# Performance work log

Measured on AMD Instinct MI355X. Metric: run time of the kernel, lower is better.

The kernel has to match this reference:

```python
import jax, jax.numpy as jnp
import numpy as np
from jax import lax

# dims
B = 1024          # batch
C_IN = 8          # board feature planes
HW = 8            # board side
FN = 16           # filter_num
SEN, INT, OUT = 1024, 2048, 1024
TOT = SEN + INT + OUT            # 4096
CNN_OUT = sum((HW - k + 1) ** 2 for k in range(1, 9)) * FN  # 204*FN = 3264
NUM_OUT = 1968
LORA_R = 64
LORA_SCALE = 128.0 / LORA_R      # alpha / rank = 2.0
TIMESTEPS = 5
DENSITY = 0.3


def setup_inputs() -> dict:
    key = jax.random.key(0)
    ks = jax.random.split(key, 20)
    inp = {"x": jax.random.normal(ks[0], (B, HW, HW, C_IN), dtype=jnp.float32)}
    # conv bank: kernels 1..8, OIHW layout
    for i, k in enumerate(range(1, 9)):
        inp[f"conv_w{k}"] = jax.random.normal(ks[1 + i], (FN, C_IN, k, k), dtype=jnp.float32) * (1.0 / np.sqrt(C_IN * k * k))
    inp["conv_b"] = jnp.zeros((8, FN), dtype=jnp.float32)
    # recurrent weight with sparsity pattern (mask = W != 0, as in register_buffer('sparsity_mask', W_init != 0))
    Wd = jax.random.normal(ks[9], (TOT, TOT), dtype=jnp.float32) * 0.02
    mask = (jax.random.uniform(ks[10], (TOT, TOT)) < DENSITY).astype(jnp.float32)
    inp["W"] = Wd * mask
    inp["lora_A"] = jax.random.normal(ks[11], (TOT, LORA_R), dtype=jnp.float32) * 0.02
    inp["lora_B"] = jax.random.normal(ks[12], (LORA_R, TOT), dtype=jnp.float32) * 0.02
    inp["ip_w"] = jax.random.normal(ks[13], (CNN_OUT, SEN), dtype=jnp.float32) * (1.0 / np.sqrt(CNN_OUT))
    inp["ip_b"] = jnp.zeros((SEN,), dtype=jnp.float32)
    inp["out_w"] = jax.random.normal(ks[14], (OUT, NUM_OUT), dtype=jnp.float32) * (1.0 / np.sqrt(OUT))
    inp["out_b"] = jnp.zeros((NUM_OUT,), dtype=jnp.float32)
    return inp


def _forward(x, conv_w1, conv_w2, conv_w3, conv_w4, conv_w5, conv_w6, conv_w7, conv_w8,
             conv_b, W, lora_A, lora_B, ip_w, ip_b, out_w, out_b):
    xn = jnp.transpose(x, (0, 3, 1, 2))  # NHWC -> NCHW, as x.permute(0,3,1,2)
    feats = []
    for i, cw in enumerate([conv_w1, conv_w2, conv_w3, conv_w4, conv_w5, conv_w6, conv_w7, conv_w8]):
        y = lax.conv_general_dilated(xn, cw, (1, 1), 'VALID',
                                     dimension_numbers=('NCHW', 'OIHW', 'NCHW'))
        y = jax.nn.relu(y + conv_b[i][None, :, None, None])  # use_relu=True
        feats.append(y.reshape(y.shape[0], -1))
    feat = jnp.concatenate(feats, axis=1)  # [B, CNN_OUT]

    # effective W with LoRA + sparsity mask
    mask = (W != 0).astype(W.dtype)
    W_eff = (W + (lora_A @ lora_B) * LORA_SCALE) * mask

    E = feat @ ip_w + ip_b                           # input_proj (no dropout: drop_out=False)
    E_pad = jnp.pad(E, ((0, 0), (0, TOT - SEN)))     # E feeds only the sensory block

    # The nine block matmuls S@Wss + I@Wrs + O@Wos etc. equal slices of state @ W_eff.
    state = jnp.zeros((x.shape[0], TOT), dtype=W.dtype)
    for t in range(TIMESTEPS):
        nxt = state @ W_eff
        if t == 0:
            nxt = nxt + E_pad
        nxt = state + nxt          # use_residual=True
        state = jax.nn.relu(nxt)

    O_state = state[:, SEN + INT:]
    return O_state @ out_w + out_b


def reference(x, conv_w1, conv_w2, conv_w3, conv_w4, conv_w5, conv_w6, conv_w7, conv_w8,
              conv_b, W, lora_A, lora_B, ip_w, ip_b, out_w, out_b):
    return _forward(x, conv_w1, conv_w2, conv_w3, conv_w4, conv_w5, conv_w6, conv_w7, conv_w8,
                    conv_b, W, lora_A, lora_B, ip_w, ip_b, out_w, out_b)
```

## Files before the change

### kernel.cpp

```cpp
#include <hip/hip_runtime.h>
#include <stdint.h>

typedef unsigned short u16;
typedef __attribute__((ext_vector_type(8))) short bf16x8;
typedef __attribute__((ext_vector_type(4))) float f32x4;

__device__ __forceinline__ u16 f2bf(float f) {
  union { float f; uint32_t u; } v; v.f = f;
  uint32_t u = v.u;
  return (u16)((u + 0x7fffu + ((u >> 16) & 1u)) >> 16);
}

__device__ __forceinline__ void gl_lds16(const void* g, void* l) {
  __builtin_amdgcn_global_load_lds(
      (const __attribute__((address_space(1))) uint32_t*)g,
      (__attribute__((address_space(3))) uint32_t*)l, 16, 0, 0);
}

__constant__ int c_off[9] = {0, 1024, 1808, 2384, 2784, 3040, 3184, 3248, 3264};

__global__ __launch_bounds__(256)
void prep_all(const float* __restrict__ x, u16* __restrict__ Xb,
              const float* __restrict__ lA, u16* __restrict__ lAb,
              const float* __restrict__ ip_w, u16* __restrict__ ip_wt,
              const float* __restrict__ out_w, u16* __restrict__ out_wt,
              const float* __restrict__ lB, u16* __restrict__ lBt,
              const float* w1, const float* w2, const float* w3, const float* w4,
              const float* w5, const float* w6, const float* w7, const float* w8,
              const float* __restrict__ cb,
              u16* __restrict__ Wct, float* __restrict__ bias_c) {
  __shared__ float tile[64][65];
  int b = blockIdx.x;
  const int t = threadIdx.x;
  if (b < 512) {
    const int i = b * 256 + t;
    const float4 v = ((const float4*)x)[i];
    ((ushort4*)Xb)[i] = make_ushort4(f2bf(v.x), f2bf(v.y), f2bf(v.z), f2bf(v.w));
    return;
  }
  b -= 512;
  if (b < 256) {
    const int i = b * 256 + t;
    const float4 v = ((const float4*)lA)[i];
    ((ushort4*)lAb)[i] = make_ushort4(f2bf(v.x), f2bf(v.y), f2bf(v.z), f2bf(v.w));
    return;
  }
  b -= 256;
  if (b < 1392) {
    const float* src; u16* dst; int R, C, bx, by;
    if (b < 816)        { src = ip_w;  dst = ip_wt;  R = 3264; C = 1024; bx = b % 16; by = b / 16; }
    else if (b < 1328)  { b -= 816;  src = out_w; dst = out_wt; R = 1024; C = 1968; bx = b % 32; by = b / 32; }
    else                { b -= 1328; src = lB;    dst = lBt;    R = 64;   C = 4096; bx = b;      by = 0; }
    const int rb = by << 6, cbs = bx << 6;
    for (int i = 0; i < 16; ++i) {
      const int idx = t + (i << 8);
      const int r = idx >> 6, c = idx & 63;
      float v = 0.f;
      if (cbs + c < C) v = src[(size_t)(rb + r) * C + cbs + c];
      tile[r][c] = v;
    }
    __syncthreads();
    const int c = t & 63, q = t >> 6;
    u16* dcol = dst + (size_t)(cbs + c) * R + rb;
    for (int v4 = 0; v4 < 4; ++v4) {
      const int r0 = (q << 4) + (v4 << 2);
      *(ushort4*)(dcol + r0) = make_ushort4(
          f2bf(tile[r0][c]), f2bf(tile[r0 + 1][c]),
          f2bf(tile[r0 + 2][c]), f2bf(tile[r0 + 3][c]));
    }
    return;
  }
  const int o = b - 1392;
  u16* row = Wct + (size_t)o * 512;
  if (t < 128) *(ushort4*)(row + (t << 2)) = make_ushort4(0, 0, 0, 0);
  if (o >= 3264) {
    if (t == 0) bias_c[o] = 0.f;
    return;
  }
  __syncthreads();
  const float* ws[8] = {w1, w2, w3, w4, w5, w6, w7, w8};
  int kidx = 0;
  while (o >= c_off[kidx + 1]) ++kidx;
  const int ks = kidx + 1;
  const int s  = 8 - kidx;
  const int r  = o - c_off[kidx];
  const int f   = r / (s * s);
  const int rem = r - f * s * s;
  const int oi  = rem / s;
  const int oj  = rem - oi * s;
  const float* w = ws[kidx] + (size_t)f * 8 * ks * ks;
  const int ne = 8 * ks * ks;
  for (int e = t; e < ne; e += 256) {
    const int c  = e / (ks * ks);
    const int er = e - c * ks * ks;
    const int di = er / ks;
    const int dj = er - di * ks;
    row[((oi + di) * 8 + (oj + dj)) * 8 + c] = f2bf(w[(c * ks + di) * ks + dj]);
  }
  if (t == 0) bias_c[o] = cb[kidx * 16 + f];
}

template<int EPI, int NR>
__device__ __forceinline__
void gemm_body(char* lds,
               const u16* __restrict__ A, int lda,
               const u16* __restrict__ Bt, int ldb, int K,
               const float* __restrict__ bias,
               const float* __restrict__ st_in, int st_ld,
               float* __restrict__ outf, int outf_ld,
               u16* __restrict__ outb, int outb_ld, int nvalid,
               int mb, int nb, int stf_c0) {
  constexpr int BN = NR * 32;
  u16 (*As)[64 * 64] = reinterpret_cast<u16 (*)[64 * 64]>(lds);
  u16 (*Bs)[BN * 64] = reinterpret_cast<u16 (*)[BN * 64]>(lds + 2 * 64 * 64 * 2);
  const int t = threadIdx.x;
  const int w = t >> 6, lane = t & 63;
  const int m0 = (w & 1) << 5, n0 = (w >> 1) * (NR << 4);
  const int lr = lane & 15, lq = lane >> 4;

  f32x4 acc[2][NR] = {};
  const int nk = K >> 6;

  auto stage = [&](int kt, int buf) {
    const int kb = kt << 6;
#pragma unroll
    for (int i = 0; i < 2; ++i) {
      const int c   = (w << 7) + (i << 6) + lane;
      const int row = c >> 3;
      const int kg  = (c & 7) ^ (row & 7);
      gl_lds16(A + (size_t)(mb + row) * lda + kb + (kg << 3),
               (char*)As[buf] + c * 16);
    }
#pragma unroll
    for (int i = 0; i < NR; ++i) {
      const int c   = w * (NR * 64) + (i << 6) + lane;
      const int row = c >> 3;
      const int kg  = (c & 7) ^ (row & 7);
      gl_lds16(Bt + (size_t)(nb + row) * ldb + kb + (kg << 3),
               (char*)Bs[buf] + c * 16);
    }
  };

  stage(0, 0);
  for (int kt = 0; kt < nk; ++kt) {
    const int buf = kt & 1;
    __syncthreads();
    if (kt + 1 < nk) stage(kt + 1, buf ^ 1);
#pragma unroll
    for (int kk = 0; kk < 2; ++kk) {
      const int kg = (kk << 2) + lq;
      const int sw = (kg ^ (lr & 7)) << 3;
      bf16x8 af[2], bf[NR];
#pragma unroll
      for (int i = 0; i < 2; ++i)
        af[i] = *(const bf16x8*)&As[buf][(m0 + (i << 4) + lr) * 64 + sw];
#pragma unroll
      for (int j = 0; j < NR; ++j)
        bf[j] = *(const bf16x8*)&Bs[buf][(n0 + (j << 4) + lr) * 64 + sw];
#pragma unroll
      for (int i = 0; i < 2; ++i)
#pragma unroll
        for (int j = 0; j < NR; ++j)
          acc[i][j] = __builtin_amdgcn_mfma_f32_16x16x32_bf16(af[i], bf[j], acc[i][j], 0, 0, 0);
    }
  }

#pragma unroll
  for (int i = 0; i < 2; ++i) {
#pragma unroll
    for (int j = 0; j < NR; ++j) {
      const int cg = nb + n0 + (j << 4) + lr;
#pragma unroll
      for (int r = 0; r < 4; ++r) {
        const int rg = mb + m0 + (i << 4) + (lq << 2) + r;
        float v = acc[i][j][r];
        if (EPI == 0) {
          outf[(size_t)rg * outf_ld + cg] = v;
        } else if (EPI == 1) {
          v += st_in[(size_t)rg * st_ld + cg];
          v = v > 0.f ? v : 0.f;
          if (cg >= stf_c0) outf[(size_t)rg * outf_ld + cg] = v;
          outb[(size_t)rg * outb_ld + cg] = f2bf(v);
        } else if (EPI == 2) {
          if (cg < nvalid)
            outf[(size_t)rg * outf_ld + cg] = v + bias[cg];
        } else {
          v += bias[cg];
          v = v > 0.f ? v : 0.f;
          outb[(size_t)rg * outb_ld + cg] = f2bf(v);
        }
      }
    }
  }
}

template<int EPI, int NR>
__global__ __launch_bounds__(256)
void gemm128(const u16* __restrict__ A, int lda,
             const u16* __restrict__ Bt, int ldb, int K,
             const float* __restrict__ bias,
             const float* __restrict__ st_in, int st_ld,
             float* __restrict__ outf, int outf_ld,
             u16* __restrict__ outb, int outb_ld, int nvalid, int stf_c0) {
  __shared__ __align__(16) char lds[2 * 64 * 64 * 2 + 2 * NR * 32 * 64 * 2];
  gemm_body<EPI, NR>(lds, A, lda, Bt, ldb, K, bias, st_in, st_ld,
                     outf, outf_ld, outb, outb_ld, nvalid,
                     blockIdx.y << 6, blockIdx.x * (NR * 32), stf_c0);
}

__global__ __launch_bounds__(256)
void weff_conv(const float* __restrict__ W, const u16* __restrict__ lBt,
               const u16* __restrict__ lAb, u16* __restrict__ Wt,
               const u16* __restrict__ Xb, const u16* __restrict__ Wct,
               const float* __restrict__ bias_c, u16* __restrict__ feat) {
  __shared__ __align__(16) char lds[49152];
  const int b = blockIdx.x;
  const int t = threadIdx.x;
  if (b < 416) {
    const int bx = b % 26, by = b / 26;
    gemm_body<3, 4>(lds, Xb, 512, Wct, 512, 512, bias_c, nullptr, 0,
                    nullptr, 0, feat, 3328, 3328, by << 6, bx << 7, 0);
    return;
  }
  u16*   As_ = (u16*)lds;
  u16*   Bs_ = (u16*)(lds + 8192);
  float* Wl  = (float*)(lds + 16384);
  u16*   Ct  = (u16*)(lds + 32768);
  const int b2 = b - 416;
  const int w = t >> 6, lane = t & 63;
  const int nb = (b2 & 63) << 6, kb = (b2 >> 6) << 6;
  const int m0 = (w & 1) << 5, n0 = (w >> 1) << 5;
  const int lr = lane & 15, lq = lane >> 4;

  for (int i = 0; i < 2; ++i) {
    const int c   = (w << 7) + (i << 6) + lane;
    const int row = c >> 3;
    const int kg  = (c & 7) ^ (row & 7);
    gl_lds16(lBt + (size_t)(nb + row) * 64 + (kg << 3), (char*)As_ + c * 16);
    gl_lds16(lAb + (size_t)(kb + row) * 64 + (kg << 3), (char*)Bs_ + c * 16);
  }
  for (int i = 0; i < 4; ++i) {
    const int c   = (w << 8) + (i << 6) + lane;
    const int row = c >> 4;
    const int cc  = (c & 15) ^ (row & 15);
    gl_lds16(W + (size_t)(kb + row) * 4096 + nb + (cc << 2), (char*)Wl + c * 16);
  }
  __syncthreads();

  f32x4 acc[2][2] = {};
  for (int kk = 0; kk < 2; ++kk) {
    const int kg = (kk << 2) + lq;
    const int sw = (kg ^ (lr & 7)) << 3;
    bf16x8 af[2], bf[2];
    for (int i = 0; i < 2; ++i)
      af[i] = *(const bf16x8*)&As_[(m0 + (i << 4) + lr) * 64 + sw];
    for (int j = 0; j < 2; ++j)
      bf[j] = *(const bf16x8*)&Bs_[(n0 + (j << 4) + lr) * 64 + sw];
    for (int i = 0; i < 2; ++i)
      for (int j = 0; j < 2; ++j)
        acc[i][j] = __builtin_amdgcn_mfma_f32_16x16x32_bf16(af[i], bf[j], acc[i][j], 0, 0, 0);
  }

  for (int i = 0; i < 2; ++i) {
    for (int j = 0; j < 2; ++j) {
      const int cg  = n0 + (j << 4) + lr;
      const int rg0 = m0 + (i << 4) + (lq << 2);
      const int ch  = (rg0 >> 2) ^ (cg & 15);
      const float4 wv4 = *(const float4*)&Wl[cg * 64 + (ch << 2)];
      const float wv[4] = {wv4.x, wv4.y, wv4.z, wv4.w};
      for (int r = 0; r < 4; ++r)
        Ct[(rg0 + r) * 68 + cg] =
            (wv[r] != 0.f) ? f2bf(wv[r] + 2.0f * acc[i][j][r]) : (u16)0;
    }
  }
  __syncthreads();

  const int row = t >> 2, kp = (t & 3) << 4;
  u16* dst = Wt + (size_t)(nb + row) * 4096 + kb + kp;
  const u16* src = &Ct[row * 68 + kp];
  for (int i = 0; i < 4; ++i)
    *(ushort4*)(dst + (i << 2)) = *(const ushort4*)(src + (i << 2));
}

__global__ __launch_bounds__(256)
void gemm_e(const u16* __restrict__ A, const u16* __restrict__ Bt,
            float* __restrict__ part) {
  __shared__ __align__(16) char lds[49152];
  const int z = blockIdx.z;
  const int k0 = z * 832;
  const int nk = (z == 3) ? 12 : 13;
  gemm_body<0, 4>(lds, A + k0, 3328, Bt + k0, 3264, nk << 6,
                  nullptr, nullptr, 0, part + ((size_t)z << 20), 1024,
                  nullptr, 0, 0, blockIdx.y << 6, blockIdx.x << 7, 0);
}

__global__ __launch_bounds__(256)
void gemm_p4(const u16* __restrict__ A, const u16* __restrict__ Bt,
             float* __restrict__ part) {
  __shared__ __align__(16) char lds[32768];
  const int z = blockIdx.z;
  gemm_body<0, 2>(lds, A + (z << 10), 4096, Bt + (z << 10), 4096, 1024,
                  nullptr, nullptr, 0, part + ((size_t)z << 20), 1024,
                  nullptr, 0, 0, blockIdx.y << 6, blockIdx.x << 6, 0);
}

__global__ __launch_bounds__(256)
void e_combine(const float* __restrict__ part, const float* __restrict__ bias,
               float* __restrict__ st_f, u16* __restrict__ st_b) {
  const int i = (blockIdx.x * 256 + threadIdx.x) << 2;
  const int row = i >> 12, col = i & 4095;
  if (col < 1024) {
    const int pi = (row << 10) + col;
    const float4 a = *(const float4*)&part[pi];
    const float4 b = *(const float4*)&part[1024 * 1024 + pi];
    const float4 c = *(const float4*)&part[2 * 1024 * 1024 + pi];
    const float4 d = *(const float4*)&part[3 * 1024 * 1024 + pi];
    const float4 bs = *(const float4*)&bias[col];
    float v[4] = {a.x + b.x + c.x + d.x + bs.x, a.y + b.y + c.y + d.y + bs.y,
                  a.z + b.z + c.z + d.z + bs.z, a.w + b.w + c.w + d.w + bs.w};
    u16 o[4];
    for (int r = 0; r < 4; ++r) {
      v[r] = v[r] > 0.f ? v[r] : 0.f;
      o[r] = f2bf(v[r]);
    }
    *(float4*)&st_f[i] = make_float4(v[0], v[1], v[2], v[3]);
    *(ushort4*)&st_b[i] = make_ushort4(o[0], o[1], o[2], o[3]);
  } else {
    *(float4*)&st_f[i] = make_float4(0.f, 0.f, 0.f, 0.f);
    *(ushort4*)&st_b[i] = make_ushort4(0, 0, 0, 0);
  }
}

__global__ __launch_bounds__(256)
void t4_combine(const float* __restrict__ part, const float* __restrict__ st_in,
                u16* __restrict__ st_b) {
  const int i = (blockIdx.x * 256 + threadIdx.x) << 2;
  const int r = i >> 10, c = i & 1023;
  const float4 a  = *(const float4*)&part[i];
  const float4 b  = *(const float4*)&part[(1 << 20) + i];
  const float4 cc = *(const float4*)&part[(2 << 20) + i];
  const float4 d  = *(const float4*)&part[(3 << 20) + i];
  const float4 s  = *(const float4*)&st_in[(size_t)r * 4096 + 3072 + c];
  float v[4] = {a.x + b.x + cc.x + d.x + s.x, a.y + b.y + cc.y + d.y + s.y,
                a.z + b.z + cc.z + d.z + s.z, a.w + b.w + cc.w + d.w + s.w};
  u16 o[4];
  for (int k = 0; k < 4; ++k) {
    v[k] = v[k] > 0.f ? v[k] : 0.f;
    o[k] = f2bf(v[k]);
  }
  *(ushort4*)&st_b[(size_t)r * 4096 + 3072 + c] = make_ushort4(o[0], o[1], o[2], o[3]);
}

extern "C" void kernel_launch(void* const* d_in, const int* in_sizes, int n_in,
                              void* d_out, int out_size, void* d_ws, size_t ws_size,
                              hipStream_t stream) {
  const float* x     = (const float*)d_in[0];
  const float* cw[8];
  for (int i = 0; i < 8; ++i) cw[i] = (const float*)d_in[1 + i];
  const float* convb = (const float*)d_in[9];
  const float* W     = (const float*)d_in[10];
  const float* lA    = (const float*)d_in[11];
  const float* lB    = (const float*)d_in[12];
  const float* ip_w  = (const float*)d_in[13];
  const float* ip_b  = (const float*)d_in[14];
  const float* out_w = (const float*)d_in[15];
  const float* out_b = (const float*)d_in[16];
  float* out = (float*)d_out;

  char* p = (char*)d_ws;
  u16* feat   = (u16*)p;  p += (size_t)1024 * 3328 * 2;
  u16* ip_wt  = (u16*)p;  p += (size_t)1024 * 3264 * 2;
  u16* out_wt = (u16*)p;  p += (size_t)2048 * 1024 * 2;
  u16* Wt     = (u16*)p;  p += (size_t)4096 * 4096 * 2;
  float* st_f[2];
  st_f[0] = (float*)p;    p += (size_t)1024 * 4096 * 4;
  st_f[1] = (float*)p;    p += (size_t)1024 * 4096 * 4;
  u16* st_b[2];
  st_b[0] = (u16*)p;      p += (size_t)1024 * 4096 * 2;
  st_b[1] = (u16*)p;      p += (size_t)1024 * 4096 * 2;

  char* q = (char*)st_f[1];
  u16* Xb       = (u16*)q;  q += (size_t)1024 * 512 * 2;
  u16* Wct      = (u16*)q;  q += (size_t)3328 * 512 * 2;
  float* bias_c = (float*)q; q += (size_t)3328 * 4;
  u16* lBt      = (u16*)q;  q += (size_t)4096 * 64 * 2;
  u16* lAb      = (u16*)q;  q += (size_t)4096 * 64 * 2;
  float* Epart  = (float*)st_f[1];
  float* Tpart  = (float*)st_f[0];

  prep_all<<<5488, 256, 0, stream>>>(x, Xb, lA, lAb, ip_w, ip_wt,
                                     out_w, out_wt, lB, lBt,
                                     cw[0], cw[1], cw[2], cw[3],
                                     cw[4], cw[5], cw[6], cw[7], convb,
                                     Wct, bias_c);

  weff_conv<<<4512, 256, 0, stream>>>(W, lBt, lAb, Wt, Xb, Wct, bias_c, feat);

  gemm_e<<<dim3(8, 16, 4), 256, 0, stream>>>(feat, ip_wt, Epart);
  e_combine<<<4096, 256, 0, stream>>>(Epart, ip_b, st_f[0], st_b[0]);

  gemm128<1, 4><<<dim3(32, 16), 256, 0, stream>>>(st_b[0], 4096, Wt, 4096, 1024,
      nullptr, st_f[0], 4096, st_f[1], 4096, st_b[1], 4096, 4096, 0);

  gemm128<1, 4><<<dim3(32, 16), 256, 0, stream>>>(st_b[1], 4096, Wt, 4096, 4096,
      nullptr, st_f[1], 4096, st_f[0], 4096, st_b[0], 4096, 4096, 0);
  gemm128<1, 4><<<dim3(32, 16), 256, 0, stream>>>(st_b[0], 4096, Wt, 4096, 4096,
      nullptr, st_f[0], 4096, st_f[1], 4096, st_b[1], 4096, 4096, 3072);

  gemm_p4<<<dim3(16, 16, 4), 256, 0, stream>>>(st_b[1],
      Wt + (size_t)3072 * 4096, Tpart);
  t4_combine<<<1024, 256, 0, stream>>>(Tpart, st_f[1], st_b[0]);

  gemm128<2, 2><<<dim3(32, 16), 256, 0, stream>>>(st_b[0] + 3072, 4096, out_wt, 1024, 1024,
      out_b, nullptr, 0, out, 1968, nullptr, 0, 1968, 0);
}
```

Before: 347.3 us.

## Fuse recurrent GEMM chain into persistent kernel with software grid barriers

Replaces the separate input-projection, combine, recurrent-step, split-K and output GEMM launches with one persistent 512-block kernel. The stages are separated by an atomic counter/generation grid barrier, which removes per-launch gaps and tail drain between dependent stages. The final recurrence step's split-K changes from four partitions of 1024 to two of 2048 so the work fits the 512-block grid. The barrier counter lives in the output buffer and assumes all 512 blocks are co-resident; if they are not, the kernel can deadlock, and the output store may race with blocks still spinning on the barrier.

```diff
diff --git a/kernel.cpp b/kernel.cpp
--- a/kernel.cpp
+++ b/kernel.cpp
@@ -28,10 +28,12 @@
               const float* w1, const float* w2, const float* w3, const float* w4,
               const float* w5, const float* w6, const float* w7, const float* w8,
               const float* __restrict__ cb,
-              u16* __restrict__ Wct, float* __restrict__ bias_c) {
+              u16* __restrict__ Wct, float* __restrict__ bias_c,
+              int* __restrict__ bar) {
   __shared__ float tile[64][65];
   int b = blockIdx.x;
   const int t = threadIdx.x;
+  if (blockIdx.x == 0 && t == 0) bar[0] = 0;
   if (b < 512) {
     const int i = b * 256 + t;
     const float4 v = ((const float4*)x)[i];
@@ -164,6 +166,7 @@
           acc[i][j] = __builtin_amdgcn_mfma_f32_16x16x32_bf16(af[i], bf[j], acc[i][j], 0, 0, 0);
     }
   }
+  __syncthreads();
 
 #pragma unroll
   for (int i = 0; i < 2; ++i) {
@@ -194,20 +197,6 @@
   }
 }
 
-template<int EPI, int NR>
-__global__ __launch_bounds__(256)
-void gemm128(const u16* __restrict__ A, int lda,
-             const u16* __restrict__ Bt, int ldb, int K,
-             const float* __restrict__ bias,
-             const float* __restrict__ st_in, int st_ld,
-             float* __restrict__ outf, int outf_ld,
-             u16* __restrict__ outb, int outb_ld, int nvalid, int stf_c0) {
-  __shared__ __align__(16) char lds[2 * 64 * 64 * 2 + 2 * NR * 32 * 64 * 2];
-  gemm_body<EPI, NR>(lds, A, lda, Bt, ldb, K, bias, st_in, st_ld,
-                     outf, outf_ld, outb, outb_ld, nvalid,
-                     blockIdx.y << 6, blockIdx.x * (NR * 32), stf_c0);
-}
-
 __global__ __launch_bounds__(256)
 void weff_conv(const float* __restrict__ W, const u16* __restrict__ lBt,
                const u16* __restrict__ lAb, u16* __restrict__ Wt,
@@ -282,73 +271,124 @@
     *(ushort4*)(dst + (i << 2)) = *(const ushort4*)(src + (i << 2));
 }
 
-__global__ __launch_bounds__(256)
-void gemm_e(const u16* __restrict__ A, const u16* __restrict__ Bt,
-            float* __restrict__ part) {
+__device__ __forceinline__ void grid_sync(int* cnt, int* gen) {
+  __syncthreads();
+  if (threadIdx.x == 0) {
+    __threadfence();
+    int g0 = __hip_atomic_load(gen, __ATOMIC_ACQUIRE, __HIP_MEMORY_SCOPE_AGENT);
+    int arrived = __hip_atomic_fetch_add(cnt, 1, __ATOMIC_ACQ_REL,
+                                         __HIP_MEMORY_SCOPE_AGENT) + 1;
+    if (arrived == 512) {
+      __hip_atomic_store(cnt, 0, __ATOMIC_RELAXED, __HIP_MEMORY_SCOPE_AGENT);
+      __hip_atomic_fetch_add(gen, 1, __ATOMIC_ACQ_REL, __HIP_MEMORY_SCOPE_AGENT);
+    } else {
+      while (__hip_atomic_load(gen, __ATOMIC_ACQUIRE,
+                               __HIP_MEMORY_SCOPE_AGENT) == g0)
+        __builtin_amdgcn_s_sleep(2);
+    }
+    __threadfence();
+  }
+  __syncthreads();
+}
+
+__global__ __launch_bounds__(256, 2)
+void mega_rec(const u16* __restrict__ feat, const u16* __restrict__ ip_wt,
+              float* __restrict__ Epart, const float* __restrict__ ip_b,
+              float* __restrict__ st_f0, u16* __restrict__ st_b0,
+              const u16* __restrict__ Wt,
+              float* __restrict__ st_f1, u16* __restrict__ st_b1,
+              float* __restrict__ Tpart, const u16* __restrict__ out_wt,
+              const float* __restrict__ out_b, float* __restrict__ outp,
+              int* bar) {
   __shared__ __align__(16) char lds[49152];
-  const int z = blockIdx.z;
-  const int k0 = z * 832;
-  const int nk = (z == 3) ? 12 : 13;
-  gemm_body<0, 4>(lds, A + k0, 3328, Bt + k0, 3264, nk << 6,
-                  nullptr, nullptr, 0, part + ((size_t)z << 20), 1024,
-                  nullptr, 0, 0, blockIdx.y << 6, blockIdx.x << 7, 0);
-}
-
-__global__ __launch_bounds__(256)
-void gemm_p4(const u16* __restrict__ A, const u16* __restrict__ Bt,
-             float* __restrict__ part) {
-  __shared__ __align__(16) char lds[32768];
-  const int z = blockIdx.z;
-  gemm_body<0, 2>(lds, A + (z << 10), 4096, Bt + (z << 10), 4096, 1024,
-                  nullptr, nullptr, 0, part + ((size_t)z << 20), 1024,
-                  nullptr, 0, 0, blockIdx.y << 6, blockIdx.x << 6, 0);
-}
-
-__global__ __launch_bounds__(256)
-void e_combine(const float* __restrict__ part, const float* __restrict__ bias,
-               float* __restrict__ st_f, u16* __restrict__ st_b) {
-  const int i = (blockIdx.x * 256 + threadIdx.x) << 2;
-  const int row = i >> 12, col = i & 4095;
-  if (col < 1024) {
-    const int pi = (row << 10) + col;
-    const float4 a = *(const float4*)&part[pi];
-    const float4 b = *(const float4*)&part[1024 * 1024 + pi];
-    const float4 c = *(const float4*)&part[2 * 1024 * 1024 + pi];
-    const float4 d = *(const float4*)&part[3 * 1024 * 1024 + pi];
-    const float4 bs = *(const float4*)&bias[col];
-    float v[4] = {a.x + b.x + c.x + d.x + bs.x, a.y + b.y + c.y + d.y + bs.y,
-                  a.z + b.z + c.z + d.z + bs.z, a.w + b.w + c.w + d.w + bs.w};
+  const int b = blockIdx.x;
+  const int t = threadIdx.x;
+  int* cnt = bar;
+  int* gen = bar + 16;
+
+  {
+    const int z = b >> 7, rem = b & 127;
+    const int k0 = z * 832;
+    const int nk = (z == 3) ? 12 : 13;
+    gemm_body<0, 4>(lds, feat + k0, 3328, ip_wt + k0, 3264, nk << 6,
+                    nullptr, nullptr, 0, Epart + ((size_t)z << 20), 1024,
+                    nullptr, 0, 0, (rem >> 3) << 6, (rem & 7) << 7, 0);
+  }
+  grid_sync(cnt, gen);
+
+  for (int idx = (b << 8) + t; idx < (1 << 20); idx += (1 << 17)) {
+    const int i = idx << 2;
+    const int row = i >> 12, col = i & 4095;
+    if (col < 1024) {
+      const int pi = (row << 10) + col;
+      const float4 a  = *(const float4*)&Epart[pi];
+      const float4 b4 = *(const float4*)&Epart[(1 << 20) + pi];
+      const float4 c4 = *(const float4*)&Epart[(2 << 20) + pi];
+      const float4 d4 = *(const float4*)&Epart[(3 << 20) + pi];
+      const float4 bs = *(const float4*)&ip_b[col];
+      float v[4] = {a.x + b4.x + c4.x + d4.x + bs.x,
+                    a.y + b4.y + c4.y + d4.y + bs.y,
+                    a.z + b4.z + c4.z + d4.z + bs.z,
+                    a.w + b4.w + c4.w + d4.w + bs.w};
+      u16 o[4];
+      for (int r = 0; r < 4; ++r) {
+        v[r] = v[r] > 0.f ? v[r] : 0.f;
+        o[r] = f2bf(v[r]);
+      }
+      *(float4*)&st_f0[i] = make_float4(v[0], v[1], v[2], v[3]);
+      *(ushort4*)&st_b0[i] = make_ushort4(o[0], o[1], o[2], o[3]);
+    } else {
+      *(float4*)&st_f0[i] = make_float4(0.f, 0.f, 0.f, 0.f);
+      *(ushort4*)&st_b0[i] = make_ushort4(0, 0, 0, 0);
+    }
+  }
+  grid_sync(cnt, gen);
+
+  gemm_body<1, 4>(lds, st_b0, 4096, Wt, 4096, 1024, nullptr, st_f0, 4096,
+                  st_f1, 4096, st_b1, 4096, 4096, (b >> 5) << 6, (b & 31) << 7, 0);
+  grid_sync(cnt, gen);
+
+  gemm_body<1, 4>(lds, st_b1, 4096, Wt, 4096, 4096, nullptr, st_f1, 4096,
+                  st_f0, 4096, st_b0, 4096, 4096, (b >> 5) << 6, (b & 31) << 7, 0);
+  grid_sync(cnt, gen);
+
+  gemm_body<1, 4>(lds, st_b0, 4096, Wt, 4096, 4096, nullptr, st_f0, 4096,
+                  st_f1, 4096, st_b1, 4096, 4096, (b >> 5) << 6, (b & 31) << 7, 3072);
+  grid_sync(cnt, gen);
+
+  {
+    const int z = b >> 8, rem = b & 255;
+    gemm_body<0, 2>(lds, st_b1 + (z << 11), 4096,
+                    Wt + (size_t)3072 * 4096 + (z << 11), 4096, 2048,
+                    nullptr, nullptr, 0, Tpart + ((size_t)z << 20), 1024,
+                    nullptr, 0, 0, (rem >> 4) << 6, (rem & 15) << 6, 0);
+  }
+  grid_sync(cnt, gen);
+
+  for (int idx = (b << 8) + t; idx < (1 << 18); idx += (1 << 17)) {
+    const int i = idx << 2;
+    const int r = i >> 10, c = i & 1023;
+    const float4 a  = *(const float4*)&Tpart[i];
+    const float4 b4 = *(const float4*)&Tpart[(1 << 20) + i];
+    const float4 s  = *(const float4*)&st_f1[(size_t)r * 4096 + 3072 + c];
+    float v[4] = {a.x + b4.x + s.x, a.y + b4.y + s.y,
+                  a.z + b4.z + s.z, a.w + b4.w + s.w};
     u16 o[4];
-    for (int r = 0; r < 4; ++r) {
-      v[r] = v[r] > 0.f ? v[r] : 0.f;
-      o[r] = f2bf(v[r]);
-    }
-    *(float4*)&st_f[i] = make_float4(v[0], v[1], v[2], v[3]);
-    *(ushort4*)&st_b[i] = make_ushort4(o[0], o[1], o[2], o[3]);
-  } else {
-    *(float4*)&st_f[i] = make_float4(0.f, 0.f, 0.f, 0.f);
-    *(ushort4*)&st_b[i] = make_ushort4(0, 0, 0, 0);
-  }
-}
-
-__global__ __launch_bounds__(256)
-void t4_combine(const float* __restrict__ part, const float* __restrict__ st_in,
-                u16* __restrict__ st_b) {
-  const int i = (blockIdx.x * 256 + threadIdx.x) << 2;
-  const int r = i >> 10, c = i & 1023;
-  const float4 a  = *(const float4*)&part[i];
-  const float4 b  = *(const float4*)&part[(1 << 20) + i];
-  const float4 cc = *(const float4*)&part[(2 << 20) + i];
-  const float4 d  = *(const float4*)&part[(3 << 20) + i];
-  const float4 s  = *(const float4*)&st_in[(size_t)r * 4096 + 3072 + c];
-  float v[4] = {a.x + b.x + cc.x + d.x + s.x, a.y + b.y + cc.y + d.y + s.y,
-                a.z + b.z + cc.z + d.z + s.z, a.w + b.w + cc.w + d.w + s.w};
-  u16 o[4];
-  for (int k = 0; k < 4; ++k) {
-    v[k] = v[k] > 0.f ? v[k] : 0.f;
-    o[k] = f2bf(v[k]);
-  }
-  *(ushort4*)&st_b[(size_t)r * 4096 + 3072 + c] = make_ushort4(o[0], o[1], o[2], o[3]);
+    for (int k = 0; k < 4; ++k) {
+      v[k] = v[k] > 0.f ? v[k] : 0.f;
+      o[k] = f2bf(v[k]);
+    }
+    *(ushort4*)&st_b0[(size_t)r * 4096 + 3072 + c] =
+        make_ushort4(o[0], o[1], o[2], o[3]);
+  }
+  grid_sync(cnt, gen);
+
+  if (b < 496) {
+    const int bx = b % 31, by = b / 31;
+    gemm_body<2, 2>(lds, st_b0 + 3072, 4096, out_wt, 1024, 1024, out_b,
+                    nullptr, 0, outp, 1968, nullptr, 0, 1968,
+                    by << 6, bx << 6, 0);
+  }
 }
 
 extern "C" void kernel_launch(void* const* d_in, const int* in_sizes, int n_in,
@@ -387,30 +427,17 @@
   u16* lAb      = (u16*)q;  q += (size_t)4096 * 64 * 2;
   float* Epart  = (float*)st_f[1];
   float* Tpart  = (float*)st_f[0];
+  int* bar      = (int*)d_out;
 
   prep_all<<<5488, 256, 0, stream>>>(x, Xb, lA, lAb, ip_w, ip_wt,
                                      out_w, out_wt, lB, lBt,
                                      cw[0], cw[1], cw[2], cw[3],
                                      cw[4], cw[5], cw[6], cw[7], convb,
-                                     Wct, bias_c);
+                                     Wct, bias_c, bar);
 
   weff_conv<<<4512, 256, 0, stream>>>(W, lBt, lAb, Wt, Xb, Wct, bias_c, feat);
 
-  gemm_e<<<dim3(8, 16, 4), 256, 0, stream>>>(feat, ip_wt, Epart);
-  e_combine<<<4096, 256, 0, stream>>>(Epart, ip_b, st_f[0], st_b[0]);
-
-  gemm128<1, 4><<<dim3(32, 16), 256, 0, stream>>>(st_b[0], 4096, Wt, 4096, 1024,
-      nullptr, st_f[0], 4096, st_f[1], 4096, st_b[1], 4096, 4096, 0);
-
-  gemm128<1, 4><<<dim3(32, 16), 256, 0, stream>>>(st_b[1], 4096, Wt, 4096, 4096,
-      nullptr, st_f[1], 4096, st_f[0], 4096, st_b[0], 4096, 4096, 0);
-  gemm128<1, 4><<<dim3(32, 16), 256, 0, stream>>>(st_b[0], 4096, Wt, 4096, 4096,
-      nullptr, st_f[0], 4096, st_f[1], 4096, st_b[1], 4096, 4096, 3072);
-
-  gemm_p4<<<dim3(16, 16, 4), 256, 0, stream>>>(st_b[1],
-      Wt + (size_t)3072 * 4096, Tpart);
-  t4_combine<<<1024, 256, 0, stream>>>(Tpart, st_f[1], st_b[0]);
-
-  gemm128<2, 2><<<dim3(32, 16), 256, 0, stream>>>(st_b[0] + 3072, 4096, out_wt, 1024, 1024,
-      out_b, nullptr, 0, out, 1968, nullptr, 0, 1968, 0);
-}
+  mega_rec<<<512, 256, 0, stream>>>(feat, ip_wt, Epart, ip_b,
+                                    st_f[0], st_b[0], Wt, st_f[1], st_b[1],
+                                    Tpart, out_wt, out_b, out, bar);
+}
```

Result: slower. 926.6 us (+166.8%).
